# Kernel optimization log

Hardware: AMD Instinct MI355X
Metric: run time of the kernel (lower is better)

## Reference

```python
import jax, jax.numpy as jnp
import numpy as np
from jax import lax

HEADS, DIM = 8, 8
T = HEADS * DIM            # total_dim = 64
C_IN, C_OUT = 256, 256
B, H, W = 8, 128, 128
BN_EPS = 1e-5


def setup_inputs() -> dict:
    key = jax.random.key(0)
    ks = jax.random.split(key, 9)
    return {
        "x": jax.random.normal(ks[0], (B, C_IN, H, W), jnp.float32),
        "W_qkv": jax.random.normal(ks[1], (3 * T, C_IN), jnp.float32) * 0.05,
        "W_p": jax.random.normal(ks[2], (3 * HEADS, DIM, DIM), jnp.float32) * 0.1,
        "W_d": jax.random.normal(ks[3], (3 * T, 1, 3, 3), jnp.float32) * 0.1,
        "W_ffn": jax.random.normal(ks[4], (C_OUT, 2 * T), jnp.float32) * 0.1,
        "bn_gamma": jax.random.uniform(ks[5], (C_OUT,), jnp.float32, 0.5, 1.5),
        "bn_beta": jax.random.normal(ks[6], (C_OUT,), jnp.float32) * 0.1,
        "bn_mean": jax.random.normal(ks[7], (C_OUT,), jnp.float32) * 0.1,
        "bn_var": jax.random.uniform(ks[8], (C_OUT,), jnp.float32, 0.5, 1.5),
    }


def reference(x, W_qkv, W_p, W_d, W_ffn, bn_gamma, bn_beta, bn_mean, bn_var):
    b, _, h, w = x.shape
    # qkv: 1x1 conv, no bias -> (B, 3T, H, W)
    qkv = jnp.einsum('bchw,oc->bohw', x, W_qkv)
    # p_conv: grouped 1x1 conv, groups = 3*heads, group size = dim
    p = qkv.reshape(b, 3 * HEADS, DIM, h, w)
    p = jnp.einsum('bgihw,goi->bgohw', p, W_p).reshape(b, 3 * T, h, w)
    # d_conv: depthwise 3x3 conv, padding 1
    d = lax.conv_general_dilated(
        p, W_d, window_strides=(1, 1), padding='SAME',
        dimension_numbers=('NCHW', 'OIHW', 'NCHW'), feature_group_count=3 * T)
    # multi-scale concat -> (B, 6T, H, W) -> (B, 2*heads, 3*dim, HW) -> (B, 2*heads, HW, 3*dim)
    g = jnp.concatenate([qkv, d], axis=1)
    g = g.reshape(b, 2 * HEADS, 3 * DIM, h * w).transpose(0, 1, 3, 2)
    q = jax.nn.relu(g[..., :DIM])
    k = jax.nn.relu(g[..., DIM:2 * DIM])
    v = g[..., 2 * DIM:]
    # padding trick: append a column of ones to v for normalization
    v1 = jnp.concatenate([v, jnp.ones(v.shape[:-1] + (1,), v.dtype)], axis=-1)
    kv = jnp.einsum('bgnd,bgne->bgde', k, v1)     # (B, 2h, dim, dim+1)
    o = jnp.einsum('bgnd,bgde->bgne', q, kv)      # (B, 2h, HW, dim+1)
    o = o[..., :DIM] / (o[..., DIM:] + 1e-15)
    o = o.transpose(0, 1, 3, 2).reshape(b, 2 * T, h, w)
    # ffn: 1x1 conv + BatchNorm (eval mode, running stats)
    y = jnp.einsum('bchw,oc->bohw', o, W_ffn)
    scale = bn_gamma / jnp.sqrt(bn_var + BN_EPS)
    return y * scale[:, None, None] + (bn_beta - bn_mean * scale)[:, None, None]
```

## Files before the change

### kernel.cpp

```cpp
#include <hip/hip_runtime.h>

#define NB    8
#define NCIN  256
#define NH    128
#define NW    128
#define NHW   16384
#define NQKV  192
#define NCOUT 256

#define K1_BK  16
#define K1_LDA 68
#define K1_LDB 260

__global__ __launch_bounds__(256) void k1_qkv(
    const float* __restrict__ x, const float* __restrict__ Wq,
    float* __restrict__ qkv)
{
  __shared__ float As[2][K1_BK][K1_LDA];
  __shared__ float Bs[2][K1_BK][K1_LDB];

  const int tid = threadIdx.x;
  const int b   = blockIdx.x >> 6;
  const int n0  = (blockIdx.x & 63) << 8;
  const int m0  = blockIdx.y << 6;

  const int am = tid >> 2;
  const int ak = (tid & 3) << 2;
  const int bk = tid >> 4;
  const int bn = (tid & 15) << 2;

  const float* aP = Wq + ((size_t)(m0 + am) << 8) + ak;
  const float* bP = x + (size_t)b * NCIN * NHW + (size_t)bk * NHW + n0 + bn;

  const int tx = tid & 31;
  const int ty = tid >> 5;

  float4 ra, rb0, rb1, rb2, rb3;
  ra  = *(const float4*)aP;
  rb0 = *(const float4*)(bP);
  rb1 = *(const float4*)(bP + 64);
  rb2 = *(const float4*)(bP + 128);
  rb3 = *(const float4*)(bP + 192);

  As[0][ak + 0][am] = ra.x;
  As[0][ak + 1][am] = ra.y;
  As[0][ak + 2][am] = ra.z;
  As[0][ak + 3][am] = ra.w;
  *(float4*)&Bs[0][bk][bn]       = rb0;
  *(float4*)&Bs[0][bk][bn + 64]  = rb1;
  *(float4*)&Bs[0][bk][bn + 128] = rb2;
  *(float4*)&Bs[0][bk][bn + 192] = rb3;
  __syncthreads();

  float acc[8][8];
#pragma unroll
  for (int i = 0; i < 8; i++)
#pragma unroll
    for (int j = 0; j < 8; j++) acc[i][j] = 0.f;

  int cur = 0;
  for (int t = 0; t < 16; ++t) {
    if (t < 15) {
      const size_t k0 = (size_t)(t + 1) * K1_BK;
      ra = *(const float4*)(aP + k0);
      const float* bq = bP + k0 * NHW;
      rb0 = *(const float4*)(bq);
      rb1 = *(const float4*)(bq + 64);
      rb2 = *(const float4*)(bq + 128);
      rb3 = *(const float4*)(bq + 192);
    }
#pragma unroll
    for (int kk = 0; kk < K1_BK; ++kk) {
      const float4 a0 = *(const float4*)&As[cur][kk][ty * 4];
      const float4 a1 = *(const float4*)&As[cur][kk][32 + ty * 4];
      const float4 b0 = *(const float4*)&Bs[cur][kk][tx * 4];
      const float4 b1 = *(const float4*)&Bs[cur][kk][128 + tx * 4];
      const float a[8]  = {a0.x, a0.y, a0.z, a0.w, a1.x, a1.y, a1.z, a1.w};
      const float bb[8] = {b0.x, b0.y, b0.z, b0.w, b1.x, b1.y, b1.z, b1.w};
#pragma unroll
      for (int i = 0; i < 8; i++)
#pragma unroll
        for (int j = 0; j < 8; j++) acc[i][j] = fmaf(a[i], bb[j], acc[i][j]);
    }
    if (t < 15) {
      const int nxt = cur ^ 1;
      As[nxt][ak + 0][am] = ra.x;
      As[nxt][ak + 1][am] = ra.y;
      As[nxt][ak + 2][am] = ra.z;
      As[nxt][ak + 3][am] = ra.w;
      *(float4*)&Bs[nxt][bk][bn]       = rb0;
      *(float4*)&Bs[nxt][bk][bn + 64]  = rb1;
      *(float4*)&Bs[nxt][bk][bn + 128] = rb2;
      *(float4*)&Bs[nxt][bk][bn + 192] = rb3;
      __syncthreads();
      cur = nxt;
    }
  }

  float* outB = qkv + (size_t)b * NQKV * NHW;
#pragma unroll
  for (int i = 0; i < 8; i++) {
    const int m = m0 + ((i < 4) ? (ty * 4 + i) : (32 + ty * 4 + (i - 4)));
    float4 v0 = {acc[i][0], acc[i][1], acc[i][2], acc[i][3]};
    float4 v1 = {acc[i][4], acc[i][5], acc[i][6], acc[i][7]};
    float* r = outB + (size_t)m * NHW + n0;
    *(float4*)(r + tx * 4)       = v0;
    *(float4*)(r + 128 + tx * 4) = v1;
  }
}

__global__ __launch_bounds__(256, 4) void k2_qkv_kv(
    const float* __restrict__ qkv, float* __restrict__ kvb)
{
  __shared__ float red[4 * 72];
  const int tid = threadIdx.x;
  const int gg  = blockIdx.y;
  const int P0  = blockIdx.x * 2048;
  const int b   = P0 >> 14;
  const int n0  = P0 & (NHW - 1);

  const float* base = qkv + ((size_t)b * NQKV + gg * 24) * NHW + n0 + tid;

  float acc[72];
#pragma unroll
  for (int i = 0; i < 72; i++) acc[i] = 0.f;

  for (int it = 0; it < 8; it++) {
    const int off = it * 256;
    float kk[8], vv[8];
#pragma unroll
    for (int j = 0; j < 8; j++) kk[j] = fmaxf(base[(size_t)(8 + j) * NHW + off], 0.f);
#pragma unroll
    for (int j = 0; j < 8; j++) vv[j] = base[(size_t)(16 + j) * NHW + off];
#pragma unroll
    for (int d = 0; d < 8; d++) {
#pragma unroll
      for (int e = 0; e < 8; e++) acc[d * 9 + e] = fmaf(kk[d], vv[e], acc[d * 9 + e]);
      acc[d * 9 + 8] += kk[d];
    }
  }

  const int wave = tid >> 6, lane = tid & 63;
#pragma unroll
  for (int i = 0; i < 72; i++) {
    float v = acc[i];
    v += __shfl_down(v, 32);
    v += __shfl_down(v, 16);
    v += __shfl_down(v, 8);
    v += __shfl_down(v, 4);
    v += __shfl_down(v, 2);
    v += __shfl_down(v, 1);
    if (lane == 0) red[wave * 72 + i] = v;
  }
  __syncthreads();
  if (tid < 72) {
    float s = red[tid] + red[72 + tid] + red[144 + tid] + red[216 + tid];
    atomicAdd(&kvb[((size_t)b * 16 + gg) * 72 + tid], s);
  }
}

#define HALO_W 34
#define HALO_H 18
#define NPOS   (HALO_W * HALO_H)

__global__ __launch_bounds__(256, 2) void k2_dw(
    const float* __restrict__ qkv, const float* __restrict__ Wp,
    const float* __restrict__ Wd, float* __restrict__ dq,
    float* __restrict__ kvb)
{
  __shared__ float pbuf[24 * NPOS];
  __shared__ float red[4 * 72];

  const int tid  = threadIdx.x;
  const int gg8  = blockIdx.y;
  const int bt   = blockIdx.x;
  const int b    = bt >> 5;
  const int tile = bt & 31;
  const int ty0  = (tile >> 2) * 16;
  const int tx0  = (tile & 3) * 32;

  const float* src = qkv + ((size_t)b * NQKV + gg8 * 24) * NHW;

  for (int idx = tid; idx < 24 * NPOS; idx += 256) {
    const int c = idx / NPOS, pos = idx % NPOS;
    const int hy = pos / HALO_W, hx = pos % HALO_W;
    const int y = ty0 + hy - 1, xx = tx0 + hx - 1;
    float v = 0.f;
    if (y >= 0 && y < NH && xx >= 0 && xx < NW) v = src[(size_t)c * NHW + y * NW + xx];
    pbuf[idx] = v;
  }
  __syncthreads();

  for (int t = tid; t < 3 * NPOS; t += 256) {
    const int gloc = t / NPOS, pos = t % NPOS;
    float qv[8];
#pragma unroll
    for (int i = 0; i < 8; i++) qv[i] = pbuf[(gloc * 8 + i) * NPOS + pos];
    const float* wp = Wp + (size_t)(gg8 * 3 + gloc) * 64;
#pragma unroll
    for (int o = 0; o < 8; o++) {
      float s = 0.f;
#pragma unroll
      for (int i = 0; i < 8; i++) s = fmaf(wp[o * 8 + i], qv[i], s);
      pbuf[(gloc * 8 + o) * NPOS + pos] = s;
    }
  }
  __syncthreads();

  float acc[72];
#pragma unroll
  for (int i = 0; i < 72; i++) acc[i] = 0.f;

  const float* wdb = Wd + (size_t)gg8 * 24 * 9;

  for (int pp = tid; pp < 512; pp += 256) {
    const int ty = pp >> 5, tx = pp & 31;
    const int n  = (ty0 + ty) * NW + (tx0 + tx);
    float kk[8], vv[8];
#pragma unroll
    for (int cc = 0; cc < 24; cc++) {
      const float* pb = pbuf + cc * NPOS + ty * HALO_W + tx;
      const float* w  = wdb + cc * 9;
      float s = 0.f;
      s = fmaf(w[0], pb[0], s);
      s = fmaf(w[1], pb[1], s);
      s = fmaf(w[2], pb[2], s);
      s = fmaf(w[3], pb[HALO_W + 0], s);
      s = fmaf(w[4], pb[HALO_W + 1], s);
      s = fmaf(w[5], pb[HALO_W + 2], s);
      s = fmaf(w[6], pb[2 * HALO_W + 0], s);
      s = fmaf(w[7], pb[2 * HALO_W + 1], s);
      s = fmaf(w[8], pb[2 * HALO_W + 2], s);
      if (cc < 8) {
        dq[((size_t)b * 64 + gg8 * 8 + cc) * NHW + n] = fmaxf(s, 0.f);
      } else if (cc < 16) {
        kk[cc - 8] = fmaxf(s, 0.f);
      } else {
        vv[cc - 16] = s;
      }
    }
#pragma unroll
    for (int d = 0; d < 8; d++) {
#pragma unroll
      for (int e = 0; e < 8; e++) acc[d * 9 + e] = fmaf(kk[d], vv[e], acc[d * 9 + e]);
      acc[d * 9 + 8] += kk[d];
    }
  }

  const int wave = tid >> 6, lane = tid & 63;
#pragma unroll
  for (int i = 0; i < 72; i++) {
    float v = acc[i];
    v += __shfl_down(v, 32);
    v += __shfl_down(v, 16);
    v += __shfl_down(v, 8);
    v += __shfl_down(v, 4);
    v += __shfl_down(v, 2);
    v += __shfl_down(v, 1);
    if (lane == 0) red[wave * 72 + i] = v;
  }
  __syncthreads();
  if (tid < 72) {
    float s = red[tid] + red[72 + tid] + red[144 + tid] + red[216 + tid];
    atomicAdd(&kvb[((size_t)b * 16 + (8 + gg8)) * 72 + tid], s);
  }
}

__global__ __launch_bounds__(256) void k3_attn_ffn(
    const float* __restrict__ qkv, const float* __restrict__ dq,
    const float* __restrict__ kvb, const float* __restrict__ Wf,
    const float* __restrict__ gamma, const float* __restrict__ beta,
    const float* __restrict__ mean, const float* __restrict__ var,
    float* __restrict__ out)
{
  __shared__ float wS[64 * 128];
  __shared__ float oS[2][8][256];

  const int tid = threadIdx.x;
  const int b   = blockIdx.x >> 6;
  const int n0  = (blockIdx.x & 63) << 8;
  const int m0  = blockIdx.y << 6;
  const int tx  = tid & 63;
  const int ty  = tid >> 6;

  {
    const float* wsrc = Wf + (size_t)m0 * 128;
#pragma unroll
    for (int i = 0; i < 8; ++i) {
      const int off = i * 1024 + tid * 4;
      *(float4*)&wS[off] = *(const float4*)&wsrc[off];
    }
  }

  float acc[16][4];
#pragma unroll
  for (int m = 0; m < 16; ++m)
#pragma unroll
    for (int p = 0; p < 4; ++p) acc[m][p] = 0.f;

  const float* kvB = kvb + (size_t)b * 16 * 72;

  for (int g = 0; g < 16; ++g) {
    const float* qp = (g < 8)
        ? qkv + ((size_t)b * NQKV + g * 24) * NHW + n0 + tid
        : dq  + ((size_t)b * 64 + (g - 8) * 8) * NHW + n0 + tid;
    float qv[8];
#pragma unroll
    for (int j = 0; j < 8; ++j) {
      const float v = qp[(size_t)j * NHW];
      qv[j] = (g < 8) ? fmaxf(v, 0.f) : v;
    }
    const float* kvg = kvB + g * 72;
    float num[9];
#pragma unroll
    for (int e = 0; e < 9; ++e) {
      float s = 0.f;
#pragma unroll
      for (int d = 0; d < 8; ++d) s = fmaf(qv[d], kvg[d * 9 + e], s);
      num[e] = s;
    }
    const float r = __builtin_amdgcn_rcpf(num[8] + 1e-15f);
    const int buf = g & 1;
#pragma unroll
    for (int e = 0; e < 8; ++e) oS[buf][e][tid] = num[e] * r;

    __syncthreads();

    float ov[4][8];
#pragma unroll
    for (int p = 0; p < 4; ++p)
#pragma unroll
      for (int e = 0; e < 8; ++e) ov[p][e] = oS[buf][e][tx + p * 64];

    const float* wrow = &wS[(ty * 16) * 128 + g * 8];
#pragma unroll
    for (int m = 0; m < 16; ++m) {
      const float4 w0 = *(const float4*)&wrow[m * 128];
      const float4 w1 = *(const float4*)&wrow[m * 128 + 4];
      const float w8[8] = {w0.x, w0.y, w0.z, w0.w, w1.x, w1.y, w1.z, w1.w};
#pragma unroll
      for (int p = 0; p < 4; ++p)
#pragma unroll
        for (int e = 0; e < 8; ++e)
          acc[m][p] = fmaf(ov[p][e], w8[e], acc[m][p]);
    }
  }

#pragma unroll
  for (int m = 0; m < 16; ++m) {
    const int oc = m0 + ty * 16 + m;
    const float sc = gamma[oc] * __builtin_amdgcn_rsqf(var[oc] + 1e-5f);
    const float bi = fmaf(-mean[oc], sc, beta[oc]);
    float* op = out + ((size_t)b * NCOUT + oc) * NHW + n0 + tx;
#pragma unroll
    for (int p = 0; p < 4; ++p) op[p * 64] = fmaf(acc[m][p], sc, bi);
  }
}

extern "C" void kernel_launch(void* const* d_in, const int* in_sizes, int n_in,
                              void* d_out, int out_size, void* d_ws, size_t ws_size,
                              hipStream_t stream) {
  const float* x     = (const float*)d_in[0];
  const float* Wq    = (const float*)d_in[1];
  const float* Wp    = (const float*)d_in[2];
  const float* Wd    = (const float*)d_in[3];
  const float* Wf    = (const float*)d_in[4];
  const float* gamma = (const float*)d_in[5];
  const float* beta  = (const float*)d_in[6];
  const float* mean  = (const float*)d_in[7];
  const float* var   = (const float*)d_in[8];
  float* out = (float*)d_out;

  char* ws = (char*)d_ws;
  float* qkv = (float*)ws;
  float* dq  = (float*)(ws + (size_t)100663296);
  float* kvb = (float*)(ws + (size_t)134217728);

  hipMemsetAsync(kvb, 0, (size_t)NB * 16 * 72 * sizeof(float), stream);

  k1_qkv<<<dim3(512, 3), 256, 0, stream>>>(x, Wq, qkv);
  k2_qkv_kv<<<dim3(64, 8), 256, 0, stream>>>(qkv, kvb);
  k2_dw<<<dim3(256, 8), 256, 0, stream>>>(qkv, Wp, Wd, dq, kvb);
  k3_attn_ffn<<<dim3(512, 4), 256, 0, stream>>>(qkv, dq, kvb, Wf, gamma, beta,
                                                mean, var, out);
}
```

Before: 725.1 us.

## Read QKV weights as wave-uniform scalar loads instead of staging in LDS

Drops the shared-memory staging of the weight tile in the QKV projection GEMM. Each wavefront now takes 16 output rows and reads weights through wave-uniform addresses (readfirstlane), so they can go through scalar loads. Each lane computes a 16x4 micro-tile instead of 8x8. This removes the LDS traffic and transposed stores for A, at the cost of scalar-load latency inside the inner loop and less reuse of each B element per thread.

Result: slower. 791.5 us (+9.2%).

```diff
diff --git a/kernel.cpp b/kernel.cpp
--- a/kernel.cpp
+++ b/kernel.cpp
@@ -9,85 +9,71 @@
 #define NCOUT 256
 
 #define K1_BK  16
-#define K1_LDA 68
 #define K1_LDB 260
 
 __global__ __launch_bounds__(256) void k1_qkv(
     const float* __restrict__ x, const float* __restrict__ Wq,
     float* __restrict__ qkv)
 {
-  __shared__ float As[2][K1_BK][K1_LDA];
   __shared__ float Bs[2][K1_BK][K1_LDB];
 
-  const int tid = threadIdx.x;
-  const int b   = blockIdx.x >> 6;
-  const int n0  = (blockIdx.x & 63) << 8;
-  const int m0  = blockIdx.y << 6;
-
-  const int am = tid >> 2;
-  const int ak = (tid & 3) << 2;
+  const int tid  = threadIdx.x;
+  const int b    = blockIdx.x >> 6;
+  const int n0   = (blockIdx.x & 63) << 8;
+  const int m0   = blockIdx.y << 6;
+  const int lane = tid & 63;
+  const int wv   = __builtin_amdgcn_readfirstlane(tid >> 6);
+
   const int bk = tid >> 4;
   const int bn = (tid & 15) << 2;
-
-  const float* aP = Wq + ((size_t)(m0 + am) << 8) + ak;
   const float* bP = x + (size_t)b * NCIN * NHW + (size_t)bk * NHW + n0 + bn;
 
-  const int tx = tid & 31;
-  const int ty = tid >> 5;
-
-  float4 ra, rb0, rb1, rb2, rb3;
-  ra  = *(const float4*)aP;
+  const float* aW = Wq + ((size_t)(m0 + wv * 16) << 8);
+
+  float4 rb0, rb1, rb2, rb3;
   rb0 = *(const float4*)(bP);
   rb1 = *(const float4*)(bP + 64);
   rb2 = *(const float4*)(bP + 128);
   rb3 = *(const float4*)(bP + 192);
-
-  As[0][ak + 0][am] = ra.x;
-  As[0][ak + 1][am] = ra.y;
-  As[0][ak + 2][am] = ra.z;
-  As[0][ak + 3][am] = ra.w;
   *(float4*)&Bs[0][bk][bn]       = rb0;
   *(float4*)&Bs[0][bk][bn + 64]  = rb1;
   *(float4*)&Bs[0][bk][bn + 128] = rb2;
   *(float4*)&Bs[0][bk][bn + 192] = rb3;
   __syncthreads();
 
-  float acc[8][8];
-#pragma unroll
-  for (int i = 0; i < 8; i++)
-#pragma unroll
-    for (int j = 0; j < 8; j++) acc[i][j] = 0.f;
+  float acc[16][4];
+#pragma unroll
+  for (int i = 0; i < 16; ++i)
+#pragma unroll
+    for (int j = 0; j < 4; ++j) acc[i][j] = 0.f;
 
   int cur = 0;
   for (int t = 0; t < 16; ++t) {
     if (t < 15) {
-      const size_t k0 = (size_t)(t + 1) * K1_BK;
-      ra = *(const float4*)(aP + k0);
-      const float* bq = bP + k0 * NHW;
+      const float* bq = bP + (size_t)(t + 1) * K1_BK * NHW;
       rb0 = *(const float4*)(bq);
       rb1 = *(const float4*)(bq + 64);
       rb2 = *(const float4*)(bq + 128);
       rb3 = *(const float4*)(bq + 192);
     }
+
+    const float* aT = aW + t * 16;
 #pragma unroll
     for (int kk = 0; kk < K1_BK; ++kk) {
-      const float4 a0 = *(const float4*)&As[cur][kk][ty * 4];
-      const float4 a1 = *(const float4*)&As[cur][kk][32 + ty * 4];
-      const float4 b0 = *(const float4*)&Bs[cur][kk][tx * 4];
-      const float4 b1 = *(const float4*)&Bs[cur][kk][128 + tx * 4];
-      const float a[8]  = {a0.x, a0.y, a0.z, a0.w, a1.x, a1.y, a1.z, a1.w};
-      const float bb[8] = {b0.x, b0.y, b0.z, b0.w, b1.x, b1.y, b1.z, b1.w};
-#pragma unroll
-      for (int i = 0; i < 8; i++)
-#pragma unroll
-        for (int j = 0; j < 8; j++) acc[i][j] = fmaf(a[i], bb[j], acc[i][j]);
-    }
+      const float4 bv = *(const float4*)&Bs[cur][kk][lane * 4];
+      const float bb[4] = {bv.x, bv.y, bv.z, bv.w};
+#pragma unroll
+      for (int i = 0; i < 16; ++i) {
+        const float a = aT[i * 256 + kk];
+        acc[i][0] = fmaf(a, bb[0], acc[i][0]);
+        acc[i][1] = fmaf(a, bb[1], acc[i][1]);
+        acc[i][2] = fmaf(a, bb[2], acc[i][2]);
+        acc[i][3] = fmaf(a, bb[3], acc[i][3]);
+      }
+    }
+
     if (t < 15) {
       const int nxt = cur ^ 1;
-      As[nxt][ak + 0][am] = ra.x;
-      As[nxt][ak + 1][am] = ra.y;
-      As[nxt][ak + 2][am] = ra.z;
-      As[nxt][ak + 3][am] = ra.w;
       *(float4*)&Bs[nxt][bk][bn]       = rb0;
       *(float4*)&Bs[nxt][bk][bn + 64]  = rb1;
       *(float4*)&Bs[nxt][bk][bn + 128] = rb2;
@@ -97,15 +83,12 @@
     }
   }
 
-  float* outB = qkv + (size_t)b * NQKV * NHW;
-#pragma unroll
-  for (int i = 0; i < 8; i++) {
-    const int m = m0 + ((i < 4) ? (ty * 4 + i) : (32 + ty * 4 + (i - 4)));
-    float4 v0 = {acc[i][0], acc[i][1], acc[i][2], acc[i][3]};
-    float4 v1 = {acc[i][4], acc[i][5], acc[i][6], acc[i][7]};
-    float* r = outB + (size_t)m * NHW + n0;
-    *(float4*)(r + tx * 4)       = v0;
-    *(float4*)(r + 128 + tx * 4) = v1;
+  float* outB = qkv + (size_t)b * NQKV * NHW + n0 + lane * 4;
+#pragma unroll
+  for (int i = 0; i < 16; ++i) {
+    const int m = m0 + wv * 16 + i;
+    float4 v = {acc[i][0], acc[i][1], acc[i][2], acc[i][3]};
+    *(float4*)(outB + (size_t)m * NHW) = v;
   }
 }
 
```
